# Performance work log

Hardware: AMD Instinct MI355X
Metric: run time of the kernel (lower is better)

Reference implementation:

```python
import jax, jax.numpy as jnp
import numpy as np

B, S, D, H = 4, 2048, 1024, 16
DH = D // H
SCALE = 1.0 / np.sqrt(DH).astype(np.float32)


def setup_inputs() -> dict:
    key = jax.random.key(0)
    k1, k2, k3 = jax.random.split(key, 3)
    x = jax.random.normal(k1, (B, S, D), dtype=jnp.float32)
    w_qkv = jax.random.normal(k2, (D, 3 * D), dtype=jnp.float32) * (1.0 / np.sqrt(D))
    b_qkv = jnp.zeros((3 * D,), dtype=jnp.float32)
    w_out = jax.random.normal(k3, (D, D), dtype=jnp.float32) * (1.0 / np.sqrt(D))
    b_out = jnp.zeros((D,), dtype=jnp.float32)
    return {"x": x, "w_qkv": w_qkv, "b_qkv": b_qkv, "w_out": w_out, "b_out": b_out}


def reference(x, w_qkv, b_qkv, w_out, b_out):
    b, s, d = x.shape
    qkv = x @ w_qkv + b_qkv                       # [b, s, 3d]
    qkv = qkv.reshape(b, s, 3, H, DH)
    qkv = jnp.transpose(qkv, (2, 0, 3, 1, 4))     # [3, b, h, s, dh]
    q, k, v = qkv[0], qkv[1], qkv[2]
    scores = jnp.einsum("bhqd,bhkd->bhqk", q, k) * SCALE
    weights = jax.nn.softmax(scores, axis=-1)
    attn = jnp.einsum("bhqk,bhkd->bhqd", weights, v)
    attn = jnp.transpose(attn, (0, 2, 1, 3)).reshape(b, s, d)
    return attn @ w_out + b_out
```

## Files before the change

### kernel.cpp

```cpp
#include <hip/hip_runtime.h>


typedef _Float16 f16;
typedef __attribute__((ext_vector_type(8))) _Float16 f16x8;
typedef __attribute__((ext_vector_type(4))) _Float16 f16x4;
typedef __attribute__((ext_vector_type(4))) float f32x4;
typedef __attribute__((ext_vector_type(16))) float f32x16;
typedef __attribute__((ext_vector_type(4))) unsigned u32x4;
typedef __attribute__((ext_vector_type(2))) int i32x2;

#define MFMA16F(a, b, c) __builtin_amdgcn_mfma_f32_16x16x32_f16((a), (b), (c), 0, 0, 0)
#define MFMA32F(a, b, c) __builtin_amdgcn_mfma_f32_32x32x16_f16((a), (b), (c), 0, 0, 0)

__device__ __forceinline__ i32x2 pl32_swap(unsigned a, unsigned b) {
  return __builtin_amdgcn_permlane32_swap((int)a, (int)b, false, false);
}

__device__ __forceinline__ void gload16(void* lds, const void* g) {
  __builtin_amdgcn_global_load_lds(
      (const __attribute__((address_space(1))) unsigned int*)g,
      (__attribute__((address_space(3))) unsigned int*)lds, 16, 0, 0);
}

__device__ __forceinline__ f16* lds_addr(f16* t, int row, int col) {
  return (f16*)((char*)t + row * 128 + ((col * 2) ^ ((row & 7) << 4)));
}
__device__ __forceinline__ f16x8 lds8(const f16* t, int row, int col) {
  return *(const f16x8*)lds_addr((f16*)t, row, col);
}

#define Q_PRESCALE 0.18033688011117f

__global__ __launch_bounds__(256) void cast_kernel(const float* __restrict__ in,
                                                   f16* __restrict__ out, int n) {
  int idx = (blockIdx.x * 256 + threadIdx.x) * 8;
  const int stride = gridDim.x * 256 * 8;
  for (; idx < n; idx += stride) {
    float v[8];
    *(float4*)&v[0] = *(const float4*)&in[idx];
    *(float4*)&v[4] = *(const float4*)&in[idx + 4];
    f16x8 h;
#pragma unroll
    for (int j = 0; j < 8; ++j) h[j] = (f16)v[j];
    *(f16x8*)&out[idx] = h;
  }
}

__global__ __launch_bounds__(256) void transpose_h_kernel(
    const float* __restrict__ in, f16* __restrict__ t_hi, int R, int C) {
  __shared__ float tile[64][65];
  const int r0 = blockIdx.y * 64;
  const int c0 = blockIdx.x * 64;
  const int tid = threadIdx.x;
  const int lr = tid >> 4;
  const int lc = (tid & 15) * 4;
#pragma unroll
  for (int i = 0; i < 4; ++i) {
    float4 v = *(const float4*)&in[(size_t)(r0 + lr + i * 16) * C + c0 + lc];
    tile[lr + i * 16][lc] = v.x;
    tile[lr + i * 16][lc + 1] = v.y;
    tile[lr + i * 16][lc + 2] = v.z;
    tile[lr + i * 16][lc + 3] = v.w;
  }
  __syncthreads();
#pragma unroll
  for (int p = 0; p < 2; ++p) {
    const int id = p * 256 + tid;
    const int oc = id >> 3;
    const int orr = (id & 7) * 8;
    f16x8 h;
#pragma unroll
    for (int j = 0; j < 8; ++j) h[j] = (f16)tile[orr + j][oc];
    *(f16x8*)&t_hi[(size_t)(c0 + oc) * R + r0 + orr] = h;
  }
}

template <int MODE>
__global__ __launch_bounds__(256, 2) void gemm_kernel(
    const f16* __restrict__ A, const f16* __restrict__ BT,
    const float* __restrict__ bias,
    f16* __restrict__ q_h, f16* __restrict__ k_h, f16* __restrict__ vt_h,
    float* __restrict__ C, int M, int N, int K) {
  __shared__ __align__(16) f16 As[2][128 * 64];
  __shared__ __align__(16) f16 Bs[2][128 * 64];

  const int tid = threadIdx.x;
  const int lane = tid & 63;
  const int wv = tid >> 6;
  const int lo16 = lane & 15;
  const int hi4 = lane >> 4;
  const int wr = wv >> 1;
  const int wc = wv & 1;
  const int m0 = blockIdx.y * 128;
  const int n0 = blockIdx.x * 128;

  f32x4 acc[4][4];
#pragma unroll
  for (int i = 0; i < 4; ++i)
#pragma unroll
    for (int j = 0; j < 4; ++j) acc[i][j] = (f32x4){0.f, 0.f, 0.f, 0.f};

  auto stage = [&](int buf, int kt) {
#pragma unroll
    for (int p = 0; p < 4; ++p) {
      const int cbase = p * 256 + wv * 64;
      const int c = cbase + lane;
      const int row = c >> 3;
      const int colc = (c & 7) ^ (row & 7);
      gload16(&As[buf][cbase * 8], &A[(size_t)(m0 + row) * K + kt + colc * 8]);
      gload16(&Bs[buf][cbase * 8], &BT[(size_t)(n0 + row) * K + kt + colc * 8]);
    }
  };

  auto compute = [&](const f16* Ac, const f16* Bc) {
#pragma unroll
    for (int ks = 0; ks < 2; ++ks) {
      f16x8 ah[4], bh[4];
#pragma unroll
      for (int t4 = 0; t4 < 4; ++t4) {
        ah[t4] = lds8((f16*)Ac, wr * 64 + t4 * 16 + lo16, ks * 32 + hi4 * 8);
        bh[t4] = lds8((f16*)Bc, wc * 64 + t4 * 16 + lo16, ks * 32 + hi4 * 8);
      }
      __builtin_amdgcn_s_setprio(1);
#pragma unroll
      for (int mt = 0; mt < 4; ++mt)
#pragma unroll
        for (int nt = 0; nt < 4; ++nt)
          acc[mt][nt] = MFMA16F(ah[mt], bh[nt], acc[mt][nt]);
      __builtin_amdgcn_s_setprio(0);
    }
  };

  stage(0, 0);
  __syncthreads();

  const int NT = K >> 6;
  for (int t = 0; t < NT; t += 2) {
    if (t + 1 < NT) stage(1, (t + 1) * 64);
    compute(As[0], Bs[0]);
    __syncthreads();
    if (t + 2 < NT) stage(0, (t + 2) * 64);
    compute(As[1], Bs[1]);
    __syncthreads();
  }

#pragma unroll
  for (int mt = 0; mt < 4; ++mt) {
    const int gmb = m0 + wr * 64 + mt * 16 + hi4 * 4;
#pragma unroll
    for (int nt = 0; nt < 4; ++nt) {
      const int gn = n0 + wc * 64 + nt * 16 + lo16;
      float v[4];
#pragma unroll
      for (int r = 0; r < 4; ++r) v[r] = acc[mt][nt][r] + bias[gn];
      if (MODE == 0) {
#pragma unroll
        for (int r = 0; r < 4; ++r) C[(size_t)(gmb + r) * N + gn] = v[r];
      } else {
        const int which = gn >> 10;
        const int h = (gn >> 6) & 15;
        const int dh = gn & 63;
        const int b = gmb >> 11;
        const int s = gmb & 2047;
        const size_t bh = (size_t)b * 16 + h;
        if (which == 0) {
#pragma unroll
          for (int r = 0; r < 4; ++r)
            q_h[(bh * 2048 + s + r) * 64 + dh] = (f16)(v[r] * Q_PRESCALE);
        } else if (which == 1) {
#pragma unroll
          for (int r = 0; r < 4; ++r)
            k_h[(bh * 2048 + s + r) * 64 + dh] = (f16)v[r];
        } else {
          f16x4 hh;
#pragma unroll
          for (int r = 0; r < 4; ++r) hh[r] = (f16)v[r];
          *(f16x4*)&vt_h[(bh * 64 + dh) * 2048 + s] = hh;
        }
      }
    }
  }
}

__global__ __launch_bounds__(256, 4) void attn_kernel(
    const f16* __restrict__ q_h, const f16* __restrict__ k_h,
    const f16* __restrict__ vt_h, f16* __restrict__ o) {
  __shared__ __align__(16) f16 Kh[2][64 * 64], Vh[2][64 * 64];

  const int tid = threadIdx.x;
  const int lane = tid & 63;
  const int wv = tid >> 6;
  const int l31 = lane & 31;
  const int h2 = lane >> 5;
  const int id0 = blockIdx.x;
  const int id = ((id0 & 7) << 7) | (id0 >> 3);
  const int bh = id >> 4;
  const int qb = id & 15;
  const size_t kvbase = (size_t)bh * 2048 * 64;
  const size_t vtbase = (size_t)bh * 64 * 2048;
  const int q0 = qb * 128 + wv * 32;

  const int c0idx = wv * 64 + lane;
  const int srow = c0idx >> 3;
  const int scol = ((c0idx & 7) ^ (srow & 7)) * 8;
  const int c1idx = 256 + wv * 64 + lane;
  const int srow1 = c1idx >> 3;
  const int scol1 = ((c1idx & 7) ^ (srow1 & 7)) * 8;

  auto stage = [&](int buf, int kv0) {
    gload16(&Kh[buf][(wv * 64) * 8], &k_h[kvbase + (size_t)(kv0 + srow) * 64 + scol]);
    gload16(&Vh[buf][(wv * 64) * 8], &vt_h[vtbase + (size_t)srow * 2048 + kv0 + scol]);
    gload16(&Kh[buf][(256 + wv * 64) * 8], &k_h[kvbase + (size_t)(kv0 + srow1) * 64 + scol1]);
    gload16(&Vh[buf][(256 + wv * 64) * 8], &vt_h[vtbase + (size_t)srow1 * 2048 + kv0 + scol1]);
  };

  f16x8 qh[4];
#pragma unroll
  for (int kt = 0; kt < 4; ++kt)
    qh[kt] = *(const f16x8*)&q_h[kvbase + (size_t)(q0 + l31) * 64 + kt * 16 + h2 * 8];

  const f16x8 ones = {(f16)1, (f16)1, (f16)1, (f16)1, (f16)1, (f16)1, (f16)1, (f16)1};

  f32x16 o_acc[2], acc_l;
#pragma unroll
  for (int i = 0; i < 16; ++i) {
    o_acc[0][i] = 0.f;
    o_acc[1][i] = 0.f;
    acc_l[i] = 0.f;
  }

  auto tile_compute = [&](const f16* Kc, const f16* Vc) {
#pragma unroll
    for (int s = 0; s < 2; ++s) {
      f32x16 sa;
#pragma unroll
      for (int i = 0; i < 16; ++i) sa[i] = 0.f;
      __builtin_amdgcn_s_setprio(1);
#pragma unroll
      for (int kt = 0; kt < 4; ++kt) {
        f16x8 kb = lds8((f16*)Kc, s * 32 + l31, kt * 16 + h2 * 8);
        sa = MFMA32F(kb, qh[kt], sa);
      }
      __builtin_amdgcn_s_setprio(0);

      unsigned w[8];
#pragma unroll
      for (int m = 0; m < 8; ++m) {
        const float pa_f = __builtin_amdgcn_exp2f(sa[2 * m]);
        const float pb_f = __builtin_amdgcn_exp2f(sa[2 * m + 1]);
        auto pk = __builtin_amdgcn_cvt_pkrtz(pa_f, pb_f);
        w[m] = __builtin_bit_cast(unsigned, pk);
      }

      f16x8 pa[2];
#pragma unroll
      for (int b = 0; b < 2; ++b) {
        const i32x2 r02 = pl32_swap(w[4 * b + 0], w[4 * b + 2]);
        const i32x2 r13 = pl32_swap(w[4 * b + 1], w[4 * b + 3]);
        u32x4 tw;
        tw[0] = (unsigned)r02[0];
        tw[1] = (unsigned)r13[0];
        tw[2] = (unsigned)r02[1];
        tw[3] = (unsigned)r13[1];
        pa[b] = __builtin_bit_cast(f16x8, tw);
      }

      __builtin_amdgcn_s_setprio(1);
#pragma unroll
      for (int b = 0; b < 2; ++b) {
        acc_l = MFMA32F(pa[b], ones, acc_l);
#pragma unroll
        for (int dt = 0; dt < 2; ++dt) {
          f16x8 vb = lds8((f16*)Vc, dt * 32 + l31, s * 32 + b * 16 + h2 * 8);
          o_acc[dt] = MFMA32F(pa[b], vb, o_acc[dt]);
        }
      }
      __builtin_amdgcn_s_setprio(0);
    }
  };

  stage(0, 0);
  __syncthreads();

  for (int t = 0; t < 32; t += 2) {
    if (t + 1 < 32) stage(1, (t + 1) * 64);
    tile_compute(Kh[0], Vh[0]);
    __syncthreads();
    if (t + 2 < 32) stage(0, (t + 2) * 64);
    tile_compute(Kh[1], Vh[1]);
    __syncthreads();
  }

  const int b_ = bh >> 4;
  const int h_ = bh & 15;
#pragma unroll
  for (int dt = 0; dt < 2; ++dt)
#pragma unroll
    for (int r = 0; r < 16; ++r) {
      const int s_row = q0 + (r & 3) + 8 * (r >> 2) + 4 * h2;
      const size_t idx =
          ((size_t)(b_ * 2048 + s_row)) * 1024 + h_ * 64 + dt * 32 + l31;
      o[idx] = (f16)(o_acc[dt][r] / acc_l[r]);
    }
}

extern "C" void kernel_launch(void* const* d_in, const int* in_sizes, int n_in,
                              void* d_out, int out_size, void* d_ws, size_t ws_size,
                              hipStream_t stream) {
  const float* x = (const float*)d_in[0];
  const float* w_qkv = (const float*)d_in[1];
  const float* b_qkv = (const float*)d_in[2];
  const float* w_out = (const float*)d_in[3];
  const float* b_out = (const float*)d_in[4];
  float* out = (float*)d_out;

  f16* ws = (f16*)d_ws;
  const size_t SZ = (size_t)64 * 2048 * 64;
  f16* q_h = ws;
  f16* k_h = ws + SZ;
  f16* vt_h = ws + 2 * SZ;
  f16* x_h = ws + 3 * SZ;
  f16* wqT_h = ws + 4 * SZ;
  f16* woT_h = wqT_h + (size_t)3072 * 1024;

  dim3 blk(256);
  cast_kernel<<<dim3(4096), blk, 0, stream>>>(x, x_h, 8 * 1024 * 1024);
  transpose_h_kernel<<<dim3(48, 16), blk, 0, stream>>>(w_qkv, wqT_h, 1024, 3072);
  transpose_h_kernel<<<dim3(16, 16), blk, 0, stream>>>(w_out, woT_h, 1024, 1024);

  gemm_kernel<1><<<dim3(24, 64), blk, 0, stream>>>(
      x_h, wqT_h, b_qkv, q_h, k_h, vt_h, nullptr, 8192, 3072, 1024);

  attn_kernel<<<dim3(1024), blk, 0, stream>>>(q_h, k_h, vt_h, x_h);

  gemm_kernel<0><<<dim3(8, 64), blk, 0, stream>>>(
      x_h, woT_h, b_out, nullptr, nullptr, nullptr, out, 8192, 1024, 1024);
}
```

Before: 193.1 us.

## Process two 32-row query sub-tiles per wave in attention to reuse K/V fragments

Each attention wave now handles 64 query rows (two 32-row sub-tiles) instead of 32, so each block covers 256 queries and the grid halves to 512 blocks. The K and V fragments read from LDS are loaded once and reused for both sub-tiles, which halves LDS reads and global K/V staging per query row. In exchange, register pressure roughly doubles for the accumulators (launch bounds drop from 4 to 2 blocks per CU) and there are fewer blocks in flight to hide latency.

```diff
diff --git a/kernel.cpp b/kernel.cpp
--- a/kernel.cpp
+++ b/kernel.cpp
@@ -182,7 +182,7 @@
   }
 }
 
-__global__ __launch_bounds__(256, 4) void attn_kernel(
+__global__ __launch_bounds__(256, 2) void attn_kernel(
     const f16* __restrict__ q_h, const f16* __restrict__ k_h,
     const f16* __restrict__ vt_h, f16* __restrict__ o) {
   __shared__ __align__(16) f16 Kh[2][64 * 64], Vh[2][64 * 64];
@@ -193,12 +193,12 @@
   const int l31 = lane & 31;
   const int h2 = lane >> 5;
   const int id0 = blockIdx.x;
-  const int id = ((id0 & 7) << 7) | (id0 >> 3);
-  const int bh = id >> 4;
-  const int qb = id & 15;
+  const int id = ((id0 & 7) << 6) | (id0 >> 3);
+  const int bh = id >> 3;
+  const int qb = id & 7;
   const size_t kvbase = (size_t)bh * 2048 * 64;
   const size_t vtbase = (size_t)bh * 64 * 2048;
-  const int q0 = qb * 128 + wv * 32;
+  const int q0 = qb * 256 + wv * 64;
 
   const int c0idx = wv * 64 + lane;
   const int srow = c0idx >> 3;
@@ -214,68 +214,88 @@
     gload16(&Vh[buf][(256 + wv * 64) * 8], &vt_h[vtbase + (size_t)srow1 * 2048 + kv0 + scol1]);
   };
 
-  f16x8 qh[4];
-#pragma unroll
-  for (int kt = 0; kt < 4; ++kt)
-    qh[kt] = *(const f16x8*)&q_h[kvbase + (size_t)(q0 + l31) * 64 + kt * 16 + h2 * 8];
+  f16x8 qh[2][4];
+#pragma unroll
+  for (int qs = 0; qs < 2; ++qs)
+#pragma unroll
+    for (int kt = 0; kt < 4; ++kt)
+      qh[qs][kt] = *(const f16x8*)&q_h[kvbase + (size_t)(q0 + qs * 32 + l31) * 64 +
+                                       kt * 16 + h2 * 8];
 
   const f16x8 ones = {(f16)1, (f16)1, (f16)1, (f16)1, (f16)1, (f16)1, (f16)1, (f16)1};
 
-  f32x16 o_acc[2], acc_l;
-#pragma unroll
-  for (int i = 0; i < 16; ++i) {
-    o_acc[0][i] = 0.f;
-    o_acc[1][i] = 0.f;
-    acc_l[i] = 0.f;
-  }
+  f32x16 o_acc[2][2], acc_l[2];
+#pragma unroll
+  for (int qs = 0; qs < 2; ++qs)
+#pragma unroll
+    for (int i = 0; i < 16; ++i) {
+      o_acc[qs][0][i] = 0.f;
+      o_acc[qs][1][i] = 0.f;
+      acc_l[qs][i] = 0.f;
+    }
 
   auto tile_compute = [&](const f16* Kc, const f16* Vc) {
 #pragma unroll
     for (int s = 0; s < 2; ++s) {
-      f32x16 sa;
-#pragma unroll
-      for (int i = 0; i < 16; ++i) sa[i] = 0.f;
+      f16x8 kb[4];
+#pragma unroll
+      for (int kt = 0; kt < 4; ++kt)
+        kb[kt] = lds8((f16*)Kc, s * 32 + l31, kt * 16 + h2 * 8);
+
+      f32x16 sa0, sa1;
+#pragma unroll
+      for (int i = 0; i < 16; ++i) {
+        sa0[i] = 0.f;
+        sa1[i] = 0.f;
+      }
       __builtin_amdgcn_s_setprio(1);
 #pragma unroll
       for (int kt = 0; kt < 4; ++kt) {
-        f16x8 kb = lds8((f16*)Kc, s * 32 + l31, kt * 16 + h2 * 8);
-        sa = MFMA32F(kb, qh[kt], sa);
+        sa0 = MFMA32F(kb[kt], qh[0][kt], sa0);
+        sa1 = MFMA32F(kb[kt], qh[1][kt], sa1);
       }
       __builtin_amdgcn_s_setprio(0);
 
-      unsigned w[8];
-#pragma unroll
-      for (int m = 0; m < 8; ++m) {
-        const float pa_f = __builtin_amdgcn_exp2f(sa[2 * m]);
-        const float pb_f = __builtin_amdgcn_exp2f(sa[2 * m + 1]);
-        auto pk = __builtin_amdgcn_cvt_pkrtz(pa_f, pb_f);
-        w[m] = __builtin_bit_cast(unsigned, pk);
-      }
-
-      f16x8 pa[2];
-#pragma unroll
-      for (int b = 0; b < 2; ++b) {
-        const i32x2 r02 = pl32_swap(w[4 * b + 0], w[4 * b + 2]);
-        const i32x2 r13 = pl32_swap(w[4 * b + 1], w[4 * b + 3]);
-        u32x4 tw;
-        tw[0] = (unsigned)r02[0];
-        tw[1] = (unsigned)r13[0];
-        tw[2] = (unsigned)r02[1];
-        tw[3] = (unsigned)r13[1];
-        pa[b] = __builtin_bit_cast(f16x8, tw);
-      }
-
-      __builtin_amdgcn_s_setprio(1);
-#pragma unroll
-      for (int b = 0; b < 2; ++b) {
-        acc_l = MFMA32F(pa[b], ones, acc_l);
-#pragma unroll
-        for (int dt = 0; dt < 2; ++dt) {
-          f16x8 vb = lds8((f16*)Vc, dt * 32 + l31, s * 32 + b * 16 + h2 * 8);
-          o_acc[dt] = MFMA32F(pa[b], vb, o_acc[dt]);
+      f16x8 vb[2][2];
+#pragma unroll
+      for (int dt = 0; dt < 2; ++dt)
+#pragma unroll
+        for (int b = 0; b < 2; ++b)
+          vb[dt][b] = lds8((f16*)Vc, dt * 32 + l31, s * 32 + b * 16 + h2 * 8);
+
+#pragma unroll
+      for (int qs = 0; qs < 2; ++qs) {
+        const f32x16& sa = qs ? sa1 : sa0;
+        unsigned w[8];
+#pragma unroll
+        for (int m = 0; m < 8; ++m) {
+          const float pa_f = __builtin_amdgcn_exp2f(sa[2 * m]);
+          const float pb_f = __builtin_amdgcn_exp2f(sa[2 * m + 1]);
+          auto pk = __builtin_amdgcn_cvt_pkrtz(pa_f, pb_f);
+          w[m] = __builtin_bit_cast(unsigned, pk);
         }
-      }
-      __builtin_amdgcn_s_setprio(0);
+        f16x8 pa[2];
+#pragma unroll
+        for (int b = 0; b < 2; ++b) {
+          const i32x2 r02 = pl32_swap(w[4 * b + 0], w[4 * b + 2]);
+          const i32x2 r13 = pl32_swap(w[4 * b + 1], w[4 * b + 3]);
+          u32x4 tw;
+          tw[0] = (unsigned)r02[0];
+          tw[1] = (unsigned)r13[0];
+          tw[2] = (unsigned)r02[1];
+          tw[3] = (unsigned)r13[1];
+          pa[b] = __builtin_bit_cast(f16x8, tw);
+        }
+        __builtin_amdgcn_s_setprio(1);
+#pragma unroll
+        for (int b = 0; b < 2; ++b) {
+          acc_l[qs] = MFMA32F(pa[b], ones, acc_l[qs]);
+#pragma unroll
+          for (int dt = 0; dt < 2; ++dt)
+            o_acc[qs][dt] = MFMA32F(pa[b], vb[dt][b], o_acc[qs][dt]);
+        }
+        __builtin_amdgcn_s_setprio(0);
+      }
     }
   };
 
@@ -294,14 +314,16 @@
   const int b_ = bh >> 4;
   const int h_ = bh & 15;
 #pragma unroll
-  for (int dt = 0; dt < 2; ++dt)
-#pragma unroll
-    for (int r = 0; r < 16; ++r) {
-      const int s_row = q0 + (r & 3) + 8 * (r >> 2) + 4 * h2;
-      const size_t idx =
-          ((size_t)(b_ * 2048 + s_row)) * 1024 + h_ * 64 + dt * 32 + l31;
-      o[idx] = (f16)(o_acc[dt][r] / acc_l[r]);
-    }
+  for (int qs = 0; qs < 2; ++qs)
+#pragma unroll
+    for (int dt = 0; dt < 2; ++dt)
+#pragma unroll
+      for (int r = 0; r < 16; ++r) {
+        const int s_row = q0 + qs * 32 + (r & 3) + 8 * (r >> 2) + 4 * h2;
+        const size_t idx =
+            ((size_t)(b_ * 2048 + s_row)) * 1024 + h_ * 64 + dt * 32 + l31;
+        o[idx] = (f16)(o_acc[qs][dt][r] / acc_l[qs][r]);
+      }
 }
 
 extern "C" void kernel_launch(void* const* d_in, const int* in_sizes, int n_in,
@@ -331,7 +353,7 @@
   gemm_kernel<1><<<dim3(24, 64), blk, 0, stream>>>(
       x_h, wqT_h, b_qkv, q_h, k_h, vt_h, nullptr, 8192, 3072, 1024);
 
-  attn_kernel<<<dim3(1024), blk, 0, stream>>>(q_h, k_h, vt_h, x_h);
+  attn_kernel<<<dim3(512), blk, 0, stream>>>(q_h, k_h, vt_h, x_h);
 
   gemm_kernel<0><<<dim3(8, 64), blk, 0, stream>>>(
       x_h, woT_h, b_out, nullptr, nullptr, nullptr, out, 8192, 1024, 1024);
```

Measured after the change: 189.6 us. No clear change (-1.9%).
